# Kernel optimization log

Hardware: AMD Instinct MI355X
Metric: run time of the kernel (lower is better)

Reference implementation:

```python
import jax, jax.numpy as jnp
import numpy as np

B, N, D, H, V, E, T = 128, 49, 512, 512, 10000, 512, 20


def setup_inputs() -> dict:
    key = jax.random.key(0)
    ks = jax.random.split(key, 12)
    s = 0.02  # weight init scale
    return {
        "img_features": jax.random.normal(ks[0], (B, N, D), jnp.float32),
        "captions": jax.random.randint(ks[1], (B, T), 0, V, jnp.int32),
        "embed": jax.random.normal(ks[2], (V, E), jnp.float32) * s,
        "W_v": jax.random.normal(ks[3], (D, D), jnp.float32) * s,
        "W_h": jax.random.normal(ks[4], (D, H), jnp.float32) * s,
        "att_b": jnp.zeros((N,), jnp.float32),
        "W_a": jax.random.normal(ks[5], (D,), jnp.float32) * s,
        "W_ih": jax.random.normal(ks[6], (4 * H, E + D), jnp.float32) * s,
        "b_ih": jnp.zeros((4 * H,), jnp.float32),
        "W_hh": jax.random.normal(ks[7], (4 * H, H), jnp.float32) * s,
        "b_hh": jnp.zeros((4 * H,), jnp.float32),
        "W_out": jax.random.normal(ks[8], (V, H), jnp.float32) * s,
        "b_out": jnp.zeros((V,), jnp.float32),
    }


def reference(img_features, captions, embed, W_v, W_h, att_b, W_a,
              W_ih, b_ih, W_hh, b_hh, W_out, b_out):
    b, n, d = img_features.shape
    t_len = captions.shape[1]
    h_dim = W_hh.shape[1]
    emb = embed[captions]                       # [B,T,E]
    mean_ctx = img_features.mean(axis=1)        # [B,D] (context at t=0)
    fv = jnp.einsum('bnd,ed->bne', img_features, W_v)  # precomputed W_v @ feats

    def step(carry, xs):
        h, c = carry
        emb_t, t = xs                           # emb_t: [B,E]
        # additive attention (computed for all t; masked out at t=0)
        oh = h @ W_h.T                          # [B,D]
        act = jax.nn.relu(fv + oh[:, None, :] + att_b[None, :, None])
        a = jax.nn.softmax(act @ W_a, axis=1)   # [B,N]
        z = jnp.einsum('bnd,bn->bd', img_features, a)
        context = jnp.where(t == 0, mean_ctx, z)
        alpha = jnp.where(t == 0, jnp.zeros_like(a), a)
        x = jnp.concatenate([context, emb_t], axis=1)   # [B, D+E]
        gates = x @ W_ih.T + b_ih + h @ W_hh.T + b_hh   # [B, 4H]
        i, f, g, o = jnp.split(gates, 4, axis=1)
        c = jax.nn.sigmoid(f) * c + jax.nn.sigmoid(i) * jnp.tanh(g)
        h = jax.nn.sigmoid(o) * jnp.tanh(c)
        out = h @ W_out.T + b_out               # [B,V]
        return (h, c), (out, alpha)

    h0 = jnp.zeros((b, h_dim), img_features.dtype)
    c0 = jnp.zeros((b, h_dim), img_features.dtype)
    _, (preds, alphas) = jax.lax.scan(
        step, (h0, c0), (emb.transpose(1, 0, 2), jnp.arange(t_len)))
    predictions = preds.transpose(1, 0, 2)      # [B,T,V]
    alphas = alphas.transpose(1, 2, 0)          # [B,N,T]
    return predictions, alphas
```

## Files before the change

kernel.cpp:

```cpp
#include <hip/hip_runtime.h>
#include <hip/hip_bf16.h>

#define BB 128
#define NN 49
#define VV 10000
#define TT 20

typedef short s8x8 __attribute__((ext_vector_type(8)));
typedef __bf16 bf8x8 __attribute__((ext_vector_type(8)));
typedef float f32x4 __attribute__((ext_vector_type(4)));

__device__ __forceinline__ float bf2f(short s){ return (float)__builtin_bit_cast(__bf16, s); }
__device__ __forceinline__ short f2bf(float f){ return __builtin_bit_cast(short, (__bf16)f); }

__device__ __forceinline__ s8x8 cast8(const float* p){
  float4 a = *(const float4*)p;
  float4 b = *(const float4*)(p + 4);
  s8x8 r;
  r[0] = f2bf(a.x); r[1] = f2bf(a.y); r[2] = f2bf(a.z); r[3] = f2bf(a.w);
  r[4] = f2bf(b.x); r[5] = f2bf(b.y); r[6] = f2bf(b.z); r[7] = f2bf(b.w);
  return r;
}

__device__ __forceinline__ f32x4 mfma16(s8x8 a, s8x8 b, f32x4 c){
  return __builtin_amdgcn_mfma_f32_16x16x32_bf16(
      __builtin_bit_cast(bf8x8, a), __builtin_bit_cast(bf8x8, b), c, 0, 0, 0);
}

__global__ __launch_bounds__(256) void k_prep2(
    const float* __restrict__ Whh, const float* __restrict__ Wih,
    const float* __restrict__ Wh,
    short* __restrict__ wcatp, short* __restrict__ whp)
{
  const long CW = 393216;
  const long CH = 32768;
  for (long c = blockIdx.x*256L + threadIdx.x; c < CW + CH; c += (long)gridDim.x*256L){
    if (c < CW){
      long s = c*8;
      int jt = (int)(s / 196608);
      int r  = (int)(s % 196608);
      int it = r >> 13;
      int r2 = r & 8191;
      int row = r2 >> 6, kk = r2 & 63;
      int jg = ((row>>5)<<9) + jt*32 + (row&31);
      int k = it*64 + kk;
      const float* src = (k < 512) ? (Whh + (long)jg*512 + k)
                                   : (Wih + (long)jg*1024 + (k - 512));
      *(s8x8*)(wcatp + s) = cast8(src);
    } else {
      long j = (c - CW)*8;
      *(s8x8*)(whp + j) = cast8(Wh + j);
    }
  }
}

__global__ __launch_bounds__(256) void k_packout(const float* __restrict__ Wout,
                                                 short* __restrict__ woutbf)
{
  for (long c = blockIdx.x*256L + threadIdx.x; c < 640000; c += (long)gridDim.x*256L)
    *(s8x8*)(woutbf + c*8) = cast8(Wout + c*8);
}

__global__ __launch_bounds__(256) void k_fv(const float* __restrict__ img,
    const float* __restrict__ Wv, const float* __restrict__ attb,
    short* __restrict__ fvbf)
{
  const int n0 = blockIdx.x*128, m0 = blockIdx.y*128;
  __shared__ short As[128*40];
  __shared__ short Bs[128*40];
  const int tid = threadIdx.x, w = tid>>6, lane = tid&63;
  f32x4 acc[8][2] = {};
  for (int k0 = 0; k0 < 512; k0 += 32){
    for (int c = tid; c < 512; c += 256){
      int row = c>>2, ko = (c&3)*8;
      *(s8x8*)(As + row*40 + ko) = cast8(img + (long)(m0+row)*512 + k0 + ko);
      *(s8x8*)(Bs + row*40 + ko) = cast8(Wv  + (long)(n0+row)*512 + k0 + ko);
    }
    __syncthreads();
    const int kb = (lane>>4)*8, l15 = lane&15;
    s8x8 b0f = *(const s8x8*)(Bs + (w*32 + l15)*40 + kb);
    s8x8 b1f = *(const s8x8*)(Bs + (w*32 + 16 + l15)*40 + kb);
    #pragma unroll
    for (int mt = 0; mt < 8; mt++){
      s8x8 a = *(const s8x8*)(As + (mt*16 + l15)*40 + kb);
      acc[mt][0] = mfma16(a, b0f, acc[mt][0]);
      acc[mt][1] = mfma16(a, b1f, acc[mt][1]);
    }
    __syncthreads();
  }
  const int l15 = lane&15;
  #pragma unroll
  for (int mt = 0; mt < 8; mt++){
    int rb = m0 + mt*16 + ((lane>>4)<<2);
    #pragma unroll
    for (int nt = 0; nt < 2; nt++){
      int cg = n0 + w*32 + nt*16 + l15;
      #pragma unroll
      for (int rr = 0; rr < 4; rr++){
        int r = rb + rr;
        fvbf[(long)r*512 + cg] = f2bf(acc[mt][nt][rr] + attb[r % NN]);
      }
    }
  }
}

__global__ __launch_bounds__(256) void k_oh(const short* __restrict__ Hcur,
    const short* __restrict__ whp, float* __restrict__ ohall)
{
  const int n0 = blockIdx.x*128;
  __shared__ short As[128*40];
  __shared__ short Bs[128*40];
  const int tid = threadIdx.x, w = tid>>6, lane = tid&63;
  f32x4 acc[8][2] = {};
  for (int k0 = 0; k0 < 512; k0 += 32){
    for (int c = tid; c < 512; c += 256){
      int row = c>>2, ko = (c&3)*8;
      *(s8x8*)(As + row*40 + ko) = *(const s8x8*)(Hcur + (long)row*512 + k0 + ko);
      *(s8x8*)(Bs + row*40 + ko) = *(const s8x8*)(whp + (long)(n0+row)*512 + k0 + ko);
    }
    __syncthreads();
    const int kb = (lane>>4)*8, l15 = lane&15;
    s8x8 b0f = *(const s8x8*)(Bs + (w*32 + l15)*40 + kb);
    s8x8 b1f = *(const s8x8*)(Bs + (w*32 + 16 + l15)*40 + kb);
    #pragma unroll
    for (int mt = 0; mt < 8; mt++){
      s8x8 a = *(const s8x8*)(As + (mt*16 + l15)*40 + kb);
      acc[mt][0] = mfma16(a, b0f, acc[mt][0]);
      acc[mt][1] = mfma16(a, b1f, acc[mt][1]);
    }
    __syncthreads();
  }
  const int l15 = lane&15;
  #pragma unroll
  for (int mt = 0; mt < 8; mt++){
    int rb = mt*16 + ((lane>>4)<<2);
    #pragma unroll
    for (int nt = 0; nt < 2; nt++){
      int cg = n0 + w*32 + nt*16 + l15;
      #pragma unroll
      for (int rr = 0; rr < 4; rr++)
        ohall[(long)(rb+rr)*512 + cg] = acc[mt][nt][rr];
    }
  }
}

__global__ __launch_bounds__(256) void k_att(const float* __restrict__ ohall,
    const short* __restrict__ fvbf, const float* __restrict__ Wa,
    const float* __restrict__ img, short* __restrict__ Cbuf,
    float* __restrict__ alph, int t)
{
  const int b = blockIdx.x, tid = threadIdx.x;
  if (t == 0){
    for (int d = tid; d < 512; d += 256){
      float s = 0.f;
      for (int n = 0; n < NN; n++) s += img[((long)b*NN + n)*512 + d];
      Cbuf[b*512 + d] = f2bf(s * (1.f/49.f));
    }
    if (tid < NN) alph[((long)b*NN + tid)*TT] = 0.f;
    return;
  }
  __shared__ float ee[64];
  __shared__ float zp[4][512];
  const int w = tid>>6, lane = tid&63;
  float ohr[8], war[8];
  {
    const float* op = ohall + b*512 + lane*8;
    const float* wp = Wa + lane*8;
    #pragma unroll
    for (int q = 0; q < 8; q++){ ohr[q] = op[q]; war[q] = wp[q]; }
  }
  for (int n = w; n < NN; n += 4){
    s8x8 v = *(const s8x8*)(fvbf + ((long)b*NN + n)*512 + lane*8);
    float s = 0.f;
    #pragma unroll
    for (int q = 0; q < 8; q++)
      s = fmaf(fmaxf(bf2f(v[q]) + ohr[q], 0.f), war[q], s);
    #pragma unroll
    for (int off = 32; off; off >>= 1) s += __shfl_xor(s, off);
    if (lane == 0) ee[n] = s;
  }
  __syncthreads();
  if (tid < 64){
    float e = (tid < NN) ? ee[tid] : -1e30f;
    float m = e;
    #pragma unroll
    for (int off = 32; off; off >>= 1) m = fmaxf(m, __shfl_xor(m, off));
    float ex = (tid < NN) ? __expf(e - m) : 0.f;
    float s = ex;
    #pragma unroll
    for (int off = 32; off; off >>= 1) s += __shfl_xor(s, off);
    float a = ex / s;
    if (tid < NN){ ee[tid] = a; alph[((long)b*NN + tid)*TT + t] = a; }
  }
  __syncthreads();
  const int cq = tid>>6, d0 = (tid&63)*8;
  float z[8] = {0,0,0,0,0,0,0,0};
  for (int n = cq; n < NN; n += 4){
    float an = ee[n];
    const float* ip = img + ((long)b*NN + n)*512 + d0;
    float4 u0 = *(const float4*)ip;
    float4 u1 = *(const float4*)(ip + 4);
    z[0] = fmaf(an, u0.x, z[0]); z[1] = fmaf(an, u0.y, z[1]);
    z[2] = fmaf(an, u0.z, z[2]); z[3] = fmaf(an, u0.w, z[3]);
    z[4] = fmaf(an, u1.x, z[4]); z[5] = fmaf(an, u1.y, z[5]);
    z[6] = fmaf(an, u1.z, z[6]); z[7] = fmaf(an, u1.w, z[7]);
  }
  #pragma unroll
  for (int q = 0; q < 8; q++) zp[cq][d0 + q] = z[q];
  __syncthreads();
  if (tid < 64){
    int dd = tid*8;
    s8x8 o;
    #pragma unroll
    for (int q = 0; q < 8; q++)
      o[q] = f2bf(zp[0][dd+q] + zp[1][dd+q] + zp[2][dd+q] + zp[3][dd+q]);
    *(s8x8*)(Cbuf + b*512 + dd) = o;
  }
}

__global__ __launch_bounds__(256) void k_gat(const short* __restrict__ Hcur,
    const short* __restrict__ Cbuf, const short* __restrict__ wcatp,
    const float* __restrict__ embed, const int* __restrict__ caps,
    const float* __restrict__ bih, const float* __restrict__ bhh,
    float* __restrict__ cst, short* __restrict__ Hnxt,
    short* __restrict__ Hall, int t)
{
  const int jt = blockIdx.x, b0 = blockIdx.y*64;
  const int J0 = jt*32;
  __shared__ short As[64*76];
  __shared__ short Bs[128*76];
  __shared__ float gs[64][132];
  const int tid = threadIdx.x, w = tid>>6, lane = tid&63;
  const long wbase = (long)jt*24*8192;

  s8x8 a_r[2], b_r[4];
  auto stage_load = [&](int it){
    #pragma unroll
    for (int i = 0; i < 2; i++){
      int c = tid + i*256;
      int row = c>>3, kkc = (c&7)*8;
      int k = it*64 + kkc, gb = b0 + row;
      s8x8 av = {0,0,0,0,0,0,0,0};
      if (k < 512){
        if (t != 0) av = *(const s8x8*)(Hcur + (long)gb*512 + k);
      } else if (k < 1024){
        av = *(const s8x8*)(Cbuf + (long)gb*512 + (k - 512));
      } else {
        av = cast8(embed + (long)caps[gb*TT + t]*512 + (k - 1024));
      }
      a_r[i] = av;
    }
    #pragma unroll
    for (int i = 0; i < 4; i++){
      long c = tid + i*256;
      b_r[i] = *(const s8x8*)(wcatp + wbase + (long)it*8192 + c*8);
    }
  };

  f32x4 acc[4][2] = {};
  stage_load(0);
  for (int it = 0; it < 24; ++it){
    #pragma unroll
    for (int i = 0; i < 2; i++){
      int c = tid + i*256;
      *(s8x8*)(As + (c>>3)*76 + (c&7)*8) = a_r[i];
    }
    #pragma unroll
    for (int i = 0; i < 4; i++){
      int c = tid + i*256;
      *(s8x8*)(Bs + (c>>3)*76 + (c&7)*8) = b_r[i];
    }
    __syncthreads();
    if (it < 23) stage_load(it + 1);
    const int kb = (lane>>4)*8, l15 = lane&15, cw = w*32;
    #pragma unroll
    for (int ks = 0; ks < 2; ks++){
      s8x8 b0f = *(const s8x8*)(Bs + (cw + l15)*76 + kb + ks*32);
      s8x8 b1f = *(const s8x8*)(Bs + (cw + 16 + l15)*76 + kb + ks*32);
      #pragma unroll
      for (int mt = 0; mt < 4; mt++){
        s8x8 a = *(const s8x8*)(As + (mt*16 + l15)*76 + kb + ks*32);
        acc[mt][0] = mfma16(a, b0f, acc[mt][0]);
        acc[mt][1] = mfma16(a, b1f, acc[mt][1]);
      }
    }
    __syncthreads();
  }
  {
    const int l15 = lane&15;
    #pragma unroll
    for (int mt = 0; mt < 4; mt++){
      int rl = mt*16 + ((lane>>4)<<2);
      #pragma unroll
      for (int nt = 0; nt < 2; nt++){
        int ct = w*32 + nt*16 + l15;
        #pragma unroll
        for (int rr = 0; rr < 4; rr++)
          gs[rl+rr][ct] = acc[mt][nt][rr];
      }
    }
  }
  __syncthreads();
  for (int task = tid; task < 2048; task += 256){
    int bl = task>>5, jc = task&31;
    int gb = b0 + bl, j = J0 + jc;
    float gi = gs[bl][jc]      + bih[j]        + bhh[j];
    float gf = gs[bl][32+jc]   + bih[512+j]    + bhh[512+j];
    float gg = gs[bl][64+jc]   + bih[1024+j]   + bhh[1024+j];
    float go = gs[bl][96+jc]   + bih[1536+j]   + bhh[1536+j];
    float ii = 1.f/(1.f+__expf(-gi));
    float ff = 1.f/(1.f+__expf(-gf));
    float e2 = __expf(2.f*gg); float g2 = (e2-1.f)/(e2+1.f);
    float oo = 1.f/(1.f+__expf(-go));
    float cp = (t == 0) ? 0.f : cst[gb*512 + j];
    float cN = ff*cp + ii*g2;
    float e3 = __expf(2.f*cN); float th = (e3-1.f)/(e3+1.f);
    float hN = oo*th;
    cst[gb*512 + j] = cN;
    short hb = f2bf(hN);
    Hnxt[gb*512 + j] = hb;
    Hall[((long)gb*TT + t)*512 + j] = hb;
  }
}

__global__ __launch_bounds__(256) void k_out(const short* __restrict__ Abf,
    const short* __restrict__ Bbf, float* __restrict__ outf,
    const float* __restrict__ bias)
{
  const int n0 = blockIdx.x*128, m0 = blockIdx.y*128;
  __shared__ short As[128*40];
  __shared__ short Bs[128*40];
  const int tid = threadIdx.x, w = tid>>6, lane = tid&63;
  f32x4 acc[8][2] = {};
  for (int k0 = 0; k0 < 512; k0 += 32){
    for (int c = tid; c < 512; c += 256){
      int row = c>>2, ko = (c&3)*8;
      *(s8x8*)(As + row*40 + ko) = *(const s8x8*)(Abf + (long)(m0+row)*512 + k0 + ko);
      int brow = n0 + row;
      s8x8 bv = {0,0,0,0,0,0,0,0};
      if (brow < VV) bv = *(const s8x8*)(Bbf + (long)brow*512 + k0 + ko);
      *(s8x8*)(Bs + row*40 + ko) = bv;
    }
    __syncthreads();
    const int kb = (lane>>4)*8, l15 = lane&15;
    s8x8 b0f = *(const s8x8*)(Bs + (w*32 + l15)*40 + kb);
    s8x8 b1f = *(const s8x8*)(Bs + (w*32 + 16 + l15)*40 + kb);
    #pragma unroll
    for (int mt = 0; mt < 8; mt++){
      s8x8 a = *(const s8x8*)(As + (mt*16 + l15)*40 + kb);
      acc[mt][0] = mfma16(a, b0f, acc[mt][0]);
      acc[mt][1] = mfma16(a, b1f, acc[mt][1]);
    }
    __syncthreads();
  }
  const int l15 = lane&15;
  #pragma unroll
  for (int mt = 0; mt < 8; mt++){
    int rb = m0 + mt*16 + ((lane>>4)<<2);
    #pragma unroll
    for (int nt = 0; nt < 2; nt++){
      int cg = n0 + w*32 + nt*16 + l15;
      if (cg >= VV) continue;
      #pragma unroll
      for (int rr = 0; rr < 4; rr++){
        int r = rb + rr;
        outf[(long)r*VV + cg] = acc[mt][nt][rr] + bias[cg];
      }
    }
  }
}

extern "C" void kernel_launch(void* const* d_in, const int* in_sizes, int n_in,
                              void* d_out, int out_size, void* d_ws, size_t ws_size,
                              hipStream_t stream)
{
  const float* img  = (const float*)d_in[0];
  const int*   caps = (const int*)d_in[1];
  const float* emb  = (const float*)d_in[2];
  const float* Wv   = (const float*)d_in[3];
  const float* Wh   = (const float*)d_in[4];
  const float* attb = (const float*)d_in[5];
  const float* Wa   = (const float*)d_in[6];
  const float* Wih  = (const float*)d_in[7];
  const float* bih  = (const float*)d_in[8];
  const float* Whh  = (const float*)d_in[9];
  const float* bhh  = (const float*)d_in[10];
  const float* Wout = (const float*)d_in[11];
  const float* bout = (const float*)d_in[12];
  float* preds = (float*)d_out;
  float* alph  = preds + (long)BB*TT*VV;

  char* ws = (char*)d_ws;
  short* wcatp  = (short*)(ws);
  short* whp    = (short*)(ws + 6291456);
  short* fvbf   = (short*)(ws + 6815744);
  short* Hbuf   = (short*)(ws + 13238272);
  short* Cbuf   = (short*)(ws + 13500416);
  float* cst    = (float*)(ws + 13631488);
  short* Hall   = (short*)(ws + 13893632);
  float* ohall  = (float*)(ws + 16515072);
  short* woutbf = (short*)(ws);

  k_prep2<<<1024, 256, 0, stream>>>(Whh, Wih, Wh, wcatp, whp);
  k_fv<<<dim3(4,49), 256, 0, stream>>>(img, Wv, attb, fvbf);

  for (int t = 0; t < TT; t++){
    short* Hc = Hbuf + (t&1)*65536;
    short* Hn = Hbuf + ((t+1)&1)*65536;
    if (t > 0)
      k_oh<<<dim3(4,1), 256, 0, stream>>>(Hc, whp, ohall);
    k_att<<<128, 256, 0, stream>>>(ohall, fvbf, Wa, img, Cbuf, alph, t);
    k_gat<<<dim3(16,2), 256, 0, stream>>>(Hc, Cbuf, wcatp, emb, caps, bih, bhh,
                                          cst, Hn, Hall, t);
  }

  k_packout<<<1024, 256, 0, stream>>>(Wout, woutbf);
  k_out<<<dim3(79,20), 256, 0, stream>>>(Hall, woutbf, preds, bout);
}
```

Measured before the change: 1.133 ms.

## Fuse h·W_h into attention, split gate GEMM finer, swizzle output GEMM

Removes the separate k_oh launch: each attention block now computes its own h·W_h^T row with a scalar dot-product loop over the bf16 weights. This saves one launch per step but makes each of the 128 blocks read the whole 512x512 weight matrix. The gate kernel now uses 16-row batch tiles, giving 128 blocks instead of 32 to raise parallelism in the latency-bound recurrence. The output GEMM also gets an XOR swizzle on its LDS tiles and an XCD-aware block remapping.

```diff
diff --git a/kernel.cpp b/kernel.cpp
--- a/kernel.cpp
+++ b/kernel.cpp
@@ -104,50 +104,10 @@
   }
 }
 
-__global__ __launch_bounds__(256) void k_oh(const short* __restrict__ Hcur,
-    const short* __restrict__ whp, float* __restrict__ ohall)
-{
-  const int n0 = blockIdx.x*128;
-  __shared__ short As[128*40];
-  __shared__ short Bs[128*40];
-  const int tid = threadIdx.x, w = tid>>6, lane = tid&63;
-  f32x4 acc[8][2] = {};
-  for (int k0 = 0; k0 < 512; k0 += 32){
-    for (int c = tid; c < 512; c += 256){
-      int row = c>>2, ko = (c&3)*8;
-      *(s8x8*)(As + row*40 + ko) = *(const s8x8*)(Hcur + (long)row*512 + k0 + ko);
-      *(s8x8*)(Bs + row*40 + ko) = *(const s8x8*)(whp + (long)(n0+row)*512 + k0 + ko);
-    }
-    __syncthreads();
-    const int kb = (lane>>4)*8, l15 = lane&15;
-    s8x8 b0f = *(const s8x8*)(Bs + (w*32 + l15)*40 + kb);
-    s8x8 b1f = *(const s8x8*)(Bs + (w*32 + 16 + l15)*40 + kb);
-    #pragma unroll
-    for (int mt = 0; mt < 8; mt++){
-      s8x8 a = *(const s8x8*)(As + (mt*16 + l15)*40 + kb);
-      acc[mt][0] = mfma16(a, b0f, acc[mt][0]);
-      acc[mt][1] = mfma16(a, b1f, acc[mt][1]);
-    }
-    __syncthreads();
-  }
-  const int l15 = lane&15;
-  #pragma unroll
-  for (int mt = 0; mt < 8; mt++){
-    int rb = mt*16 + ((lane>>4)<<2);
-    #pragma unroll
-    for (int nt = 0; nt < 2; nt++){
-      int cg = n0 + w*32 + nt*16 + l15;
-      #pragma unroll
-      for (int rr = 0; rr < 4; rr++)
-        ohall[(long)(rb+rr)*512 + cg] = acc[mt][nt][rr];
-    }
-  }
-}
-
-__global__ __launch_bounds__(256) void k_att(const float* __restrict__ ohall,
-    const short* __restrict__ fvbf, const float* __restrict__ Wa,
-    const float* __restrict__ img, short* __restrict__ Cbuf,
-    float* __restrict__ alph, int t)
+__global__ __launch_bounds__(256) void k_att(const short* __restrict__ Hcur,
+    const short* __restrict__ whp, const short* __restrict__ fvbf,
+    const float* __restrict__ Wa, const float* __restrict__ img,
+    short* __restrict__ Cbuf, float* __restrict__ alph, int t)
 {
   const int b = blockIdx.x, tid = threadIdx.x;
   if (t == 0){
@@ -159,15 +119,29 @@
     if (tid < NN) alph[((long)b*NN + tid)*TT] = 0.f;
     return;
   }
+  __shared__ float hs[512];
+  __shared__ float ohs[512];
   __shared__ float ee[64];
   __shared__ float zp[4][512];
+  for (int d = tid; d < 512; d += 256) hs[d] = bf2f(Hcur[b*512 + d]);
+  __syncthreads();
+  for (int d = tid; d < 512; d += 256){
+    const short* wr = whp + (long)d*512;
+    float s = 0.f;
+    for (int j8 = 0; j8 < 512; j8 += 8){
+      s8x8 v = *(const s8x8*)(wr + j8);
+      #pragma unroll
+      for (int q = 0; q < 8; q++) s = fmaf(hs[j8+q], bf2f(v[q]), s);
+    }
+    ohs[d] = s;
+  }
+  __syncthreads();
   const int w = tid>>6, lane = tid&63;
   float ohr[8], war[8];
   {
-    const float* op = ohall + b*512 + lane*8;
     const float* wp = Wa + lane*8;
     #pragma unroll
-    for (int q = 0; q < 8; q++){ ohr[q] = op[q]; war[q] = wp[q]; }
+    for (int q = 0; q < 8; q++){ ohr[q] = ohs[lane*8 + q]; war[q] = wp[q]; }
   }
   for (int n = w; n < NN; n += 4){
     s8x8 v = *(const s8x8*)(fvbf + ((long)b*NN + n)*512 + lane*8);
@@ -225,20 +199,18 @@
     float* __restrict__ cst, short* __restrict__ Hnxt,
     short* __restrict__ Hall, int t)
 {
-  const int jt = blockIdx.x, b0 = blockIdx.y*64;
+  const int jt = blockIdx.x, b0 = blockIdx.y*16;
   const int J0 = jt*32;
-  __shared__ short As[64*76];
+  __shared__ short As[16*76];
   __shared__ short Bs[128*76];
-  __shared__ float gs[64][132];
+  __shared__ float gs[16][132];
   const int tid = threadIdx.x, w = tid>>6, lane = tid&63;
   const long wbase = (long)jt*24*8192;
 
-  s8x8 a_r[2], b_r[4];
+  s8x8 a_r, b_r[4];
   auto stage_load = [&](int it){
-    #pragma unroll
-    for (int i = 0; i < 2; i++){
-      int c = tid + i*256;
-      int row = c>>3, kkc = (c&7)*8;
+    if (tid < 128){
+      int row = tid>>3, kkc = (tid&7)*8;
       int k = it*64 + kkc, gb = b0 + row;
       s8x8 av = {0,0,0,0,0,0,0,0};
       if (k < 512){
@@ -248,7 +220,7 @@
       } else {
         av = cast8(embed + (long)caps[gb*TT + t]*512 + (k - 1024));
       }
-      a_r[i] = av;
+      a_r = av;
     }
     #pragma unroll
     for (int i = 0; i < 4; i++){
@@ -257,14 +229,11 @@
     }
   };
 
-  f32x4 acc[4][2] = {};
+  f32x4 acc[2] = {};
   stage_load(0);
   for (int it = 0; it < 24; ++it){
-    #pragma unroll
-    for (int i = 0; i < 2; i++){
-      int c = tid + i*256;
-      *(s8x8*)(As + (c>>3)*76 + (c&7)*8) = a_r[i];
-    }
+    if (tid < 128)
+      *(s8x8*)(As + (tid>>3)*76 + (tid&7)*8) = a_r;
     #pragma unroll
     for (int i = 0; i < 4; i++){
       int c = tid + i*256;
@@ -277,31 +246,25 @@
     for (int ks = 0; ks < 2; ks++){
       s8x8 b0f = *(const s8x8*)(Bs + (cw + l15)*76 + kb + ks*32);
       s8x8 b1f = *(const s8x8*)(Bs + (cw + 16 + l15)*76 + kb + ks*32);
-      #pragma unroll
-      for (int mt = 0; mt < 4; mt++){
-        s8x8 a = *(const s8x8*)(As + (mt*16 + l15)*76 + kb + ks*32);
-        acc[mt][0] = mfma16(a, b0f, acc[mt][0]);
-        acc[mt][1] = mfma16(a, b1f, acc[mt][1]);
-      }
+      s8x8 a = *(const s8x8*)(As + l15*76 + kb + ks*32);
+      acc[0] = mfma16(a, b0f, acc[0]);
+      acc[1] = mfma16(a, b1f, acc[1]);
     }
     __syncthreads();
   }
   {
     const int l15 = lane&15;
-    #pragma unroll
-    for (int mt = 0; mt < 4; mt++){
-      int rl = mt*16 + ((lane>>4)<<2);
+    int rl = (lane>>4)<<2;
+    #pragma unroll
+    for (int nt = 0; nt < 2; nt++){
+      int ct = w*32 + nt*16 + l15;
       #pragma unroll
-      for (int nt = 0; nt < 2; nt++){
-        int ct = w*32 + nt*16 + l15;
-        #pragma unroll
-        for (int rr = 0; rr < 4; rr++)
-          gs[rl+rr][ct] = acc[mt][nt][rr];
-      }
-    }
-  }
-  __syncthreads();
-  for (int task = tid; task < 2048; task += 256){
+      for (int rr = 0; rr < 4; rr++)
+        gs[rl+rr][ct] = acc[nt][rr];
+    }
+  }
+  __syncthreads();
+  for (int task = tid; task < 512; task += 256){
     int bl = task>>5, jc = task&31;
     int gb = b0 + bl, j = J0 + jc;
     float gi = gs[bl][jc]      + bih[j]        + bhh[j];
@@ -327,7 +290,10 @@
     const short* __restrict__ Bbf, float* __restrict__ outf,
     const float* __restrict__ bias)
 {
-  const int n0 = blockIdx.x*128, m0 = blockIdx.y*128;
+  int flat = blockIdx.y*79 + blockIdx.x;
+  int xcd = flat & 7, idx = flat >> 3;
+  int wg = (xcd < 4) ? xcd*198 + idx : 792 + (xcd-4)*197 + idx;
+  const int n0 = (wg/20)*128, m0 = (wg%20)*128;
   __shared__ short As[128*40];
   __shared__ short Bs[128*40];
   const int tid = threadIdx.x, w = tid>>6, lane = tid&63;
@@ -335,14 +301,16 @@
   for (int k0 = 0; k0 < 512; k0 += 32){
     for (int c = tid; c < 512; c += 256){
       int row = c>>2, ko = (c&3)*8;
-      *(s8x8*)(As + row*40 + ko) = *(const s8x8*)(Abf + (long)(m0+row)*512 + k0 + ko);
+      int kos = ((c&3) ^ (row&3))*8;
+      *(s8x8*)(As + row*40 + kos) = *(const s8x8*)(Abf + (long)(m0+row)*512 + k0 + ko);
       int brow = n0 + row;
       s8x8 bv = {0,0,0,0,0,0,0,0};
       if (brow < VV) bv = *(const s8x8*)(Bbf + (long)brow*512 + k0 + ko);
-      *(s8x8*)(Bs + row*40 + ko) = bv;
-    }
-    __syncthreads();
-    const int kb = (lane>>4)*8, l15 = lane&15;
+      *(s8x8*)(Bs + row*40 + kos) = bv;
+    }
+    __syncthreads();
+    const int l15 = lane&15;
+    const int kb = (((lane>>4) ^ (l15&3)))*8;
     s8x8 b0f = *(const s8x8*)(Bs + (w*32 + l15)*40 + kb);
     s8x8 b1f = *(const s8x8*)(Bs + (w*32 + 16 + l15)*40 + kb);
     #pragma unroll
@@ -398,7 +366,6 @@
   short* Cbuf   = (short*)(ws + 13500416);
   float* cst    = (float*)(ws + 13631488);
   short* Hall   = (short*)(ws + 13893632);
-  float* ohall  = (float*)(ws + 16515072);
   short* woutbf = (short*)(ws);
 
   k_prep2<<<1024, 256, 0, stream>>>(Whh, Wih, Wh, wcatp, whp);
@@ -407,10 +374,8 @@
   for (int t = 0; t < TT; t++){
     short* Hc = Hbuf + (t&1)*65536;
     short* Hn = Hbuf + ((t+1)&1)*65536;
-    if (t > 0)
-      k_oh<<<dim3(4,1), 256, 0, stream>>>(Hc, whp, ohall);
-    k_att<<<128, 256, 0, stream>>>(ohall, fvbf, Wa, img, Cbuf, alph, t);
-    k_gat<<<dim3(16,2), 256, 0, stream>>>(Hc, Cbuf, wcatp, emb, caps, bih, bhh,
+    k_att<<<128, 256, 0, stream>>>(Hc, whp, fvbf, Wa, img, Cbuf, alph, t);
+    k_gat<<<dim3(16,8), 256, 0, stream>>>(Hc, Cbuf, wcatp, emb, caps, bih, bhh,
                                           cst, Hn, Hall, t);
   }
 
```

Result: faster. 974.1 us (-14.0%).
